# Performance work log

Measured on AMD Instinct MI355X. Metric: run time of the kernel, lower is better.

## Reference

```python
import jax, jax.numpy as jnp
import numpy as np

DIM = 512
NUM_HEADS = 8
HEAD_DIM = DIM // NUM_HEADS        # 64
L_HEADS = 4                        # int(8 * 0.5)
H_HEADS = NUM_HEADS - L_HEADS      # 4
L_DIM = L_HEADS * HEAD_DIM         # 256
H_DIM = H_HEADS * HEAD_DIM         # 256
WS = 2                             # window_size
SCALE = HEAD_DIM ** -0.5
SEQ_LEN = 1024


def setup_inputs() -> dict:
    key = jax.random.key(0)
    ks = jax.random.split(key, 13)
    B, N, C = 16, 1024, DIM
    def w(k, shape, fan_in):
        return (jax.random.normal(k, shape, jnp.float32) / np.sqrt(fan_in)).astype(jnp.float32)
    return {
        "x": jax.random.normal(ks[0], (B, N, C), jnp.float32),
        "pos_emb": jax.random.normal(ks[1], (1, SEQ_LEN, C), jnp.float32) * 0.02,
        "l_q_w": w(ks[2], (C, L_DIM), C),
        "l_kv_w": w(ks[3], (C, 2 * L_DIM), C),
        "l_proj_w": w(ks[4], (L_DIM, L_DIM), L_DIM),
        "l_proj_b": jax.random.normal(ks[5], (L_DIM,), jnp.float32) * 0.01,
        "h_qkv_w": w(ks[6], (C, 3 * H_DIM), C),
        "h_proj_w": w(ks[7], (H_DIM, H_DIM), H_DIM),
        "h_proj_b": jax.random.normal(ks[8], (H_DIM,), jnp.float32) * 0.01,
        "in_proj_w": w(ks[9], (C, 3 * C), C),
        "in_proj_b": jax.random.normal(ks[10], (3 * C,), jnp.float32) * 0.01,
        "out_proj_w": w(ks[11], (C, C), C),
        "out_proj_b": jax.random.normal(ks[12], (C,), jnp.float32) * 0.01,
        "H": 32,
        "W": 32,
    }


def _hifi(xg, h_qkv_w, h_proj_w, h_proj_b, H, W):
    B, _, _, C = xg.shape
    hg, wg = H // WS, W // WS
    G, T = hg * wg, WS * WS
    # [B, hg, WS, wg, WS, C] -> [B, G, T, C] (window partition)
    xw = xg.reshape(B, hg, WS, wg, WS, C).transpose(0, 1, 3, 2, 4, 5).reshape(B, G, T, C)
    qkv = (xw @ h_qkv_w).reshape(B, G, T, 3, H_HEADS, HEAD_DIM)
    q = qkv[:, :, :, 0].transpose(0, 1, 3, 2, 4)  # [B,G,h,T,d]
    k = qkv[:, :, :, 1].transpose(0, 1, 3, 2, 4)
    v = qkv[:, :, :, 2].transpose(0, 1, 3, 2, 4)
    attn = jax.nn.softmax(jnp.einsum("bghtd,bghsd->bghts", q, k) * SCALE, axis=-1)
    o = jnp.einsum("bghts,bghsd->bghtd", attn, v)
    # window un-partition: [B,G,h,T,d] -> [B,H,W,h_dim]
    o = o.transpose(0, 1, 3, 2, 4).reshape(B, hg, wg, WS, WS, H_DIM)
    o = o.transpose(0, 1, 3, 2, 4, 5).reshape(B, H, W, H_DIM)
    return o @ h_proj_w + h_proj_b


def _lofi(xg, l_q_w, l_kv_w, l_proj_w, l_proj_b, H, W):
    B, _, _, C = xg.shape
    N = H * W
    q = (xg @ l_q_w).reshape(B, N, L_HEADS, HEAD_DIM)
    kv = (xg @ l_kv_w).reshape(B, N, 2, L_HEADS, HEAD_DIM)
    k, v = kv[:, :, 0], kv[:, :, 1]
    attn = jax.nn.softmax(jnp.einsum("bnhd,bmhd->bhnm", q, k) * SCALE, axis=-1)
    o = jnp.einsum("bhnm,bmhd->bnhd", attn, v).reshape(B, H, W, L_DIM)
    return o @ l_proj_w + l_proj_b


def _mha(y, in_proj_w, in_proj_b, out_proj_w, out_proj_b):
    B, N, C = y.shape
    qkv = y @ in_proj_w + in_proj_b
    q, k, v = jnp.split(qkv, 3, axis=-1)
    q = q.reshape(B, N, NUM_HEADS, HEAD_DIM)
    k = k.reshape(B, N, NUM_HEADS, HEAD_DIM)
    v = v.reshape(B, N, NUM_HEADS, HEAD_DIM)
    attn = jax.nn.softmax(jnp.einsum("bnhd,bmhd->bhnm", q, k) * SCALE, axis=-1)
    o = jnp.einsum("bhnm,bmhd->bnhd", attn, v).reshape(B, N, C)
    return o @ out_proj_w + out_proj_b


def reference(x, pos_emb, l_q_w, l_kv_w, l_proj_w, l_proj_b,
              h_qkv_w, h_proj_w, h_proj_b,
              in_proj_w, in_proj_b, out_proj_w, out_proj_b, H, W):
    B, N, C = x.shape
    x = x + pos_emb[:, :N, :]
    xg = x.reshape(B, H, W, C)
    hifi_out = _hifi(xg, h_qkv_w, h_proj_w, h_proj_b, H, W)
    lofi_out = _lofi(xg, l_q_w, l_kv_w, l_proj_w, l_proj_b, H, W)
    y = jnp.concatenate([hifi_out, lofi_out], axis=-1).reshape(B, N, C)
    return _mha(y, in_proj_w, in_proj_b, out_proj_w, out_proj_b)
```

## Files before the change

### kernel.cpp

```cpp
#include <hip/hip_runtime.h>

typedef unsigned short ushort_t;
typedef short bf16x8 __attribute__((ext_vector_type(8)));
typedef float f32x4 __attribute__((ext_vector_type(4)));
typedef float f32x16 __attribute__((ext_vector_type(16)));

#define DEV __device__ __forceinline__

DEV ushort_t f2bf(float f) {
  return (ushort_t)((__float_as_uint(f) + 0x8000u) >> 16);
}
DEV unsigned pk_bf16(float lo, float hi) {
  unsigned a = __float_as_uint(lo) + 0x8000u;
  unsigned b = __float_as_uint(hi) + 0x8000u;
  return __builtin_amdgcn_perm(b, a, 0x07060302);
}
DEV unsigned cvtpk_bf16(float lo, float hi) {
  unsigned r;
  asm("v_cvt_pk_bf16_f32 %0, %1, %2" : "=v"(r) : "v"(lo), "v"(hi));
  return r;
}
DEV float bf2f(ushort_t h) {
  union { unsigned int u; float f; } v; v.u = ((unsigned int)h) << 16;
  return v.f;
}
DEV f32x4 mfma16(bf16x8 a, bf16x8 b, f32x4 c) {
  return __builtin_amdgcn_mfma_f32_16x16x32_bf16(a, b, c, 0, 0, 0);
}
DEV f32x16 mfma32(bf16x8 a, bf16x8 b, f32x16 c) {
  return __builtin_amdgcn_mfma_f32_32x32x16_bf16(a, b, c, 0, 0, 0);
}
DEV void pl32swap(unsigned &a, unsigned &b) {
  asm("v_permlane32_swap_b32 %0, %1" : "+v"(a), "+v"(b));
}
typedef __attribute__((address_space(3))) void lds_void;
typedef const __attribute__((address_space(1))) void glb_void;
DEV void gl_lds16(const void* g, void* l) {
  __builtin_amdgcn_global_load_lds((glb_void*)g, (lds_void*)l, 16, 0, 0);
}

__global__ __launch_bounds__(256)
void gemm_bt(const ushort_t* __restrict__ A, int lda,
             const ushort_t* __restrict__ BT,
             const float* __restrict__ bias,
             ushort_t* __restrict__ Cb, float* __restrict__ Cf,
             int ldc, int coff, int K, float scv, int sc_lo, int sc_hi)
{
  __shared__ __align__(16) ushort_t As[128 * 32];
  __shared__ __align__(16) ushort_t Bs[128 * 32];
  const int tid  = threadIdx.x;
  const int wave = tid >> 6, lane = tid & 63;
  const int quad = lane >> 4, r16 = lane & 15;
  const int nwg = gridDim.x * gridDim.y;
  const int lin = blockIdx.x + gridDim.x * blockIdx.y;
  const int logical = (lin & 7) * (nwg >> 3) + (lin >> 3);
  const int nbn = gridDim.y;
  const int mb = logical / nbn, nb = logical - mb * nbn;
  const int m0 = mb * 128, n0 = nb * 128;
  const int wm = (wave >> 1) * 64, wn = (wave & 1) * 64;

  f32x4 acc[4][4];
#pragma unroll
  for (int i = 0; i < 4; ++i)
#pragma unroll
    for (int j = 0; j < 4; ++j) acc[i][j] = (f32x4){0.f, 0.f, 0.f, 0.f};

  for (int kc = 0; kc < K; kc += 32) {
#pragma unroll
    for (int p = 0; p < 4; ++p) {
      int wp = p * 4 + wave;
      int lc = ((wp & 7) << 6) + lane;
      int row = lc >> 2, e8 = (lc & 3) * 8;
      if (wp < 8) gl_lds16(&A[(size_t)(m0 + row) * lda + kc + e8], &As[lc * 8]);
      else        gl_lds16(&BT[(size_t)(n0 + row) * K  + kc + e8], &Bs[lc * 8]);
    }
    __syncthreads();
    bf16x8 af[4], bfr[4];
#pragma unroll
    for (int i = 0; i < 4; ++i) {
      af[i]  = *(const bf16x8*)&As[(wm + i * 16 + r16) * 32 + quad * 8];
      bfr[i] = *(const bf16x8*)&Bs[(wn + i * 16 + r16) * 32 + quad * 8];
    }
#pragma unroll
    for (int mi = 0; mi < 4; ++mi)
#pragma unroll
      for (int ni = 0; ni < 4; ++ni)
        acc[mi][ni] = mfma16(af[mi], bfr[ni], acc[mi][ni]);
    __syncthreads();
  }

#pragma unroll
  for (int mi = 0; mi < 4; ++mi) {
#pragma unroll
    for (int ni = 0; ni < 4; ++ni) {
      int col = n0 + wn + ni * 16 + r16;
      float bv = bias ? bias[col] : 0.f;
      float s = (col >= sc_lo && col < sc_hi) ? scv : 1.0f;
#pragma unroll
      for (int r = 0; r < 4; ++r) {
        int row = m0 + wm + mi * 16 + quad * 4 + r;
        float v = (acc[mi][ni][r] + bv) * s;
        if (Cf) Cf[(size_t)row * ldc + coff + col] = v;
        else    Cb[(size_t)row * ldc + coff + col] = f2bf(v);
      }
    }
  }
}

__global__ __launch_bounds__(256)
void gemm_proj(const ushort_t* __restrict__ rB,
               const ushort_t* __restrict__ hT, const ushort_t* __restrict__ lT,
               const float* __restrict__ hb, const float* __restrict__ lb,
               ushort_t* __restrict__ y)
{
  __shared__ __align__(16) ushort_t As[128 * 32];
  __shared__ __align__(16) ushort_t Bs[128 * 32];
  const int tid  = threadIdx.x;
  const int wave = tid >> 6, lane = tid & 63;
  const int quad = lane >> 4, r16 = lane & 15;
  const int lin = blockIdx.x + 128 * blockIdx.y;
  const int logical = (lin & 7) * 64 + (lin >> 3);
  const int nidx = logical & 3, m0 = (logical >> 2) * 128;
  const int sel = nidx >> 1, n0 = (nidx & 1) * 128;
  const ushort_t* A  = rB + sel * 256;
  const ushort_t* BT = sel ? lT : hT;
  const float* bias  = sel ? lb : hb;
  const int coff = sel * 256;
  const int wm = (wave >> 1) * 64, wn = (wave & 1) * 64;

  f32x4 acc[4][4];
#pragma unroll
  for (int i = 0; i < 4; ++i)
#pragma unroll
    for (int j = 0; j < 4; ++j) acc[i][j] = (f32x4){0.f, 0.f, 0.f, 0.f};

  for (int kc = 0; kc < 256; kc += 32) {
#pragma unroll
    for (int p = 0; p < 4; ++p) {
      int wp = p * 4 + wave;
      int lc = ((wp & 7) << 6) + lane;
      int row = lc >> 2, e8 = (lc & 3) * 8;
      if (wp < 8) gl_lds16(&A[(size_t)(m0 + row) * 512 + kc + e8], &As[lc * 8]);
      else        gl_lds16(&BT[(size_t)(n0 + row) * 256 + kc + e8], &Bs[lc * 8]);
    }
    __syncthreads();
    bf16x8 af[4], bfr[4];
#pragma unroll
    for (int i = 0; i < 4; ++i) {
      af[i]  = *(const bf16x8*)&As[(wm + i * 16 + r16) * 32 + quad * 8];
      bfr[i] = *(const bf16x8*)&Bs[(wn + i * 16 + r16) * 32 + quad * 8];
    }
#pragma unroll
    for (int mi = 0; mi < 4; ++mi)
#pragma unroll
      for (int ni = 0; ni < 4; ++ni)
        acc[mi][ni] = mfma16(af[mi], bfr[ni], acc[mi][ni]);
    __syncthreads();
  }

#pragma unroll
  for (int mi = 0; mi < 4; ++mi) {
#pragma unroll
    for (int ni = 0; ni < 4; ++ni) {
      int col = n0 + wn + ni * 16 + r16;
      float bv = bias[col];
#pragma unroll
      for (int r = 0; r < 4; ++r) {
        int row = m0 + wm + mi * 16 + quad * 4 + r;
        y[(size_t)row * 512 + coff + col] = f2bf(acc[mi][ni][r] + bv);
      }
    }
  }
}

template<int QG>
__global__ __launch_bounds__(256, 2)
void flash_attn9(const ushort_t* __restrict__ Q, int qs, int q_ch,
                 const ushort_t* __restrict__ Kg, int ks, int k_ch,
                 const ushort_t* __restrict__ vT,
                 ushort_t* __restrict__ O, int os, int o_ch,
                 int N)
{
  __shared__ __align__(16) ushort_t Ks[2][64 * 64];
  __shared__ __align__(16) ushort_t Vs[2][64 * 64];

  const int H = gridDim.y;
  const int tid = threadIdx.x, wave = tid >> 6, lane = tid & 63;
  const int c = lane & 31, hh = lane >> 5;

  const int nwg = gridDim.x * H * gridDim.z;
  const int lin = blockIdx.x + gridDim.x * (blockIdx.y + H * blockIdx.z);
  const int logical = (lin & 7) * (nwg >> 3) + (lin >> 3);
  const int QBS = 8 / QG;
  const int qb = logical & (QBS - 1);
  const int t8 = logical / QBS;
  const int b = (H == 8) ? (t8 >> 3) : (t8 >> 2);
  const int h = t8 - b * H;
  const int q0 = qb * (128 * QG) + wave * (32 * QG);

  bf16x8 qf[QG][4];
#pragma unroll
  for (int qg = 0; qg < QG; ++qg) {
    const ushort_t* qp =
        Q + ((size_t)b * N + q0 + qg * 32 + c) * qs + q_ch + h * 64 + hh * 8;
#pragma unroll
    for (int s = 0; s < 4; ++s) qf[qg][s] = *(const bf16x8*)&qp[s * 16];
  }
  const ushort_t* kbase = Kg + ((size_t)b * N) * ks + k_ch + h * 64;
  const ushort_t* vbase = vT + ((size_t)(b * H + h) * 64) * N;

  f32x16 oacc[QG][2];
#pragma unroll
  for (int qg = 0; qg < QG; ++qg)
#pragma unroll
    for (int i = 0; i < 16; ++i) { oacc[qg][0][i] = 0.f; oacc[qg][1][i] = 0.f; }
  float l_acc[QG];
#pragma unroll
  for (int qg = 0; qg < QG; ++qg) l_acc[qg] = 0.f;

  auto stage = [&](int s0, int buf) {
#pragma unroll
    for (int p = 0; p < 4; ++p) {
      int wp = p * 4 + wave;
      int lc = ((wp & 7) << 6) + lane;
      int row = lc >> 3, cc = lc & 7;
      int e8 = ((cc ^ (row & 7)) * 8);
      if (wp < 8) gl_lds16(kbase + (size_t)(s0 + row) * ks + e8, &Ks[buf][lc * 8]);
      else        gl_lds16(vbase + (size_t)row * N + s0 + e8,    &Vs[buf][lc * 8]);
    }
  };

  stage(0, 0);
  const int NT = N >> 6;
  for (int it = 0; it < NT; ++it) {
    const int cur = it & 1;
    __syncthreads();
    if (it + 1 < NT) stage((it + 1) << 6, cur ^ 1);

    bf16x8 Bf[QG][4];
#pragma unroll
    for (int kb = 0; kb < 2; ++kb) {
      const int krow = kb * 32 + c;
      const ushort_t* kr = &Ks[cur][krow * 64];
      bf16x8 kf[4];
#pragma unroll
      for (int s = 0; s < 4; ++s)
        kf[s] = *(const bf16x8*)&kr[(((s << 1) + hh) ^ (krow & 7)) * 8];

#pragma unroll
      for (int qg = 0; qg < QG; ++qg) {
        f32x16 z;
#pragma unroll
        for (int i = 0; i < 16; ++i) z[i] = 0.f;
#pragma unroll
        for (int s = 0; s < 4; ++s) z = mfma32(kf[s], qf[qg][s], z);
        float ts = 0.f;
        unsigned W[8];
#pragma unroll
        for (int t = 0; t < 8; ++t) {
          float p0 = __builtin_amdgcn_exp2f(z[2 * t]);
          float p1 = __builtin_amdgcn_exp2f(z[2 * t + 1]);
          ts += p0 + p1;
          W[t] = cvtpk_bf16(p0, p1);
        }
        l_acc[qg] += ts;
        union U8 { bf16x8 f; unsigned u[4]; } f0, f1;
        unsigned a0 = W[0], b0 = W[2]; pl32swap(a0, b0);
        unsigned a1 = W[1], b1 = W[3]; pl32swap(a1, b1);
        f0.u[0] = a0; f0.u[1] = a1; f0.u[2] = b0; f0.u[3] = b1;
        unsigned a2 = W[4], b2 = W[6]; pl32swap(a2, b2);
        unsigned a3 = W[5], b3 = W[7]; pl32swap(a3, b3);
        f1.u[0] = a2; f1.u[1] = a3; f1.u[2] = b2; f1.u[3] = b3;
        Bf[qg][kb * 2]     = f0.f;
        Bf[qg][kb * 2 + 1] = f1.f;
      }
    }

#pragma unroll
    for (int db = 0; db < 2; ++db) {
      const int vrow = db * 32 + c;
      const ushort_t* vr = &Vs[cur][vrow * 64];
      bf16x8 vf[4];
#pragma unroll
      for (int s = 0; s < 4; ++s)
        vf[s] = *(const bf16x8*)&vr[(((s << 1) + hh) ^ (vrow & 7)) * 8];
#pragma unroll
      for (int qg = 0; qg < QG; ++qg)
#pragma unroll
        for (int s = 0; s < 4; ++s)
          oacc[qg][db] = mfma32(vf[s], Bf[qg][s], oacc[qg][db]);
    }
  }

#pragma unroll
  for (int qg = 0; qg < QG; ++qg) {
    float l = l_acc[qg] + __shfl_xor(l_acc[qg], 32);
    float inv = 1.f / l;
    ushort_t* op = O + ((size_t)b * N + q0 + qg * 32 + c) * os + o_ch + h * 64;
#pragma unroll
    for (int db = 0; db < 2; ++db) {
#pragma unroll
      for (int g = 0; g < 4; ++g) {
        uint2 pkv;
        pkv.x = cvtpk_bf16(oacc[qg][db][4 * g + 0] * inv, oacc[qg][db][4 * g + 1] * inv);
        pkv.y = cvtpk_bf16(oacc[qg][db][4 * g + 2] * inv, oacc[qg][db][4 * g + 3] * inv);
        *(uint2*)&op[db * 32 + g * 8 + hh * 4] = pkv;
      }
    }
  }
}

__global__ __launch_bounds__(256)
void transpose_v(const ushort_t* __restrict__ in, int ld, int ch,
                 ushort_t* __restrict__ out, int N, int H)
{
  __shared__ __align__(16) ushort_t T[64][72];
  const int s0 = blockIdx.x * 64, h = blockIdx.y, b = blockIdx.z;
  const int tid = threadIdx.x;
#pragma unroll
  for (int p = 0; p < 2; ++p) {
    int c = p * 256 + tid;
    int sr = c >> 3, d0 = (c & 7) * 8;
    *(uint4*)&T[sr][d0] =
        *(const uint4*)&in[((size_t)b * N + s0 + sr) * ld + ch + h * 64 + d0];
  }
  __syncthreads();
  const int d = tid >> 2, sp = (tid & 3) * 16;
  union { uint4 v; ushort_t u[8]; } A, B;
#pragma unroll
  for (int j = 0; j < 8; ++j) { A.u[j] = T[sp + j][d]; B.u[j] = T[sp + 8 + j][d]; }
  ushort_t* op = out + ((size_t)(b * H + h) * 64 + d) * N + s0 + sp;
  *(uint4*)&op[0] = A.v;
  *(uint4*)&op[8] = B.v;
}

__global__ __launch_bounds__(256)
void hifi_win(const ushort_t* __restrict__ qkv, int ld, ushort_t* __restrict__ out)
{
  const int bg = blockIdx.x;
  const int b = bg >> 8, g = bg & 255;
  const int head = threadIdx.x >> 6, lane = threadIdx.x & 63;
  const int gh = g >> 4, gw = g & 15;

  int n[4];
  float q[4], k[4], v[4];
#pragma unroll
  for (int t = 0; t < 4; ++t) {
    n[t] = (gh * 2 + (t >> 1)) * 32 + gw * 2 + (t & 1);
    size_t base = ((size_t)b * 1024 + n[t]) * ld + head * 64 + lane;
    q[t] = bf2f(qkv[base]);
    k[t] = bf2f(qkv[base + 256]);
    v[t] = bf2f(qkv[base + 512]);
  }
  float sc[4][4];
#pragma unroll
  for (int t = 0; t < 4; ++t)
#pragma unroll
    for (int s = 0; s < 4; ++s) {
      float p = q[t] * k[s];
#pragma unroll
      for (int off = 32; off >= 1; off >>= 1) p += __shfl_xor(p, off);
      sc[t][s] = p * 0.125f;
    }
#pragma unroll
  for (int t = 0; t < 4; ++t) {
    float m = fmaxf(fmaxf(sc[t][0], sc[t][1]), fmaxf(sc[t][2], sc[t][3]));
    float p0 = __expf(sc[t][0] - m), p1 = __expf(sc[t][1] - m);
    float p2 = __expf(sc[t][2] - m), p3 = __expf(sc[t][3] - m);
    float sum = p0 + p1 + p2 + p3;
    float o = (p0 * v[0] + p1 * v[1] + p2 * v[2] + p3 * v[3]) / sum;
    out[((size_t)b * 1024 + n[t]) * 512 + head * 64 + lane] = f2bf(o);
  }
}

struct WEnt { const float* W; ushort_t* WT; int K; int N; };
struct WArgs { WEnt e[7]; };

__global__ __launch_bounds__(256)
void w_prep(WArgs a)
{
  WEnt w = a.e[blockIdx.z];
  if ((int)blockIdx.x >= (w.K >> 6) || (int)blockIdx.y >= (w.N >> 6)) return;
  __shared__ float T[64][65];
  const int k0 = blockIdx.x * 64, n0 = blockIdx.y * 64;
  const int tid = threadIdx.x;
#pragma unroll
  for (int p = 0; p < 4; ++p) {
    int c = p * 256 + tid;
    int kr = c >> 4, f4 = (c & 15) * 4;
    float4 v = *(const float4*)&w.W[(size_t)(k0 + kr) * w.N + n0 + f4];
    T[f4 + 0][kr] = v.x; T[f4 + 1][kr] = v.y;
    T[f4 + 2][kr] = v.z; T[f4 + 3][kr] = v.w;
  }
  __syncthreads();
  const int nl = tid >> 2, kp = (tid & 3) * 16;
  union { uint4 v; ushort_t u[8]; } A, B;
#pragma unroll
  for (int j = 0; j < 8; ++j) {
    A.u[j] = f2bf(T[nl][kp + j]);
    B.u[j] = f2bf(T[nl][kp + 8 + j]);
  }
  ushort_t* op = w.WT + (size_t)(n0 + nl) * w.K + k0 + kp;
  *(uint4*)&op[0] = A.v;
  *(uint4*)&op[8] = B.v;
}

__global__ void add_pos(const float* __restrict__ x, const float* __restrict__ pos,
                        ushort_t* __restrict__ xpe)
{
  int idx = blockIdx.x * 256 + threadIdx.x;
  int e = idx * 4;
  float4 xv = *(const float4*)&x[e];
  float4 pv = *(const float4*)&pos[e & (512 * 1024 - 1)];
  uint2 pk;
  pk.x = pk_bf16(xv.x + pv.x, xv.y + pv.y);
  pk.y = pk_bf16(xv.z + pv.z, xv.w + pv.w);
  *(uint2*)&xpe[e] = pk;
}

extern "C" void kernel_launch(void* const* d_in, const int* in_sizes, int n_in,
                              void* d_out, int out_size, void* d_ws, size_t ws_size,
                              hipStream_t stream)
{
  const float* x         = (const float*)d_in[0];
  const float* pos       = (const float*)d_in[1];
  const float* l_q_w     = (const float*)d_in[2];
  const float* l_kv_w    = (const float*)d_in[3];
  const float* l_proj_w  = (const float*)d_in[4];
  const float* l_proj_b  = (const float*)d_in[5];
  const float* h_qkv_w   = (const float*)d_in[6];
  const float* h_proj_w  = (const float*)d_in[7];
  const float* h_proj_b  = (const float*)d_in[8];
  const float* in_proj_w = (const float*)d_in[9];
  const float* in_proj_b = (const float*)d_in[10];
  const float* out_proj_w= (const float*)d_in[11];
  const float* out_proj_b= (const float*)d_in[12];
  float* out = (float*)d_out;

  const float QSCALE = 0.125f * 1.44269504f;

  char* ws = (char*)d_ws;
  ushort_t* xpe = (ushort_t*)(ws);
  ushort_t* y   = (ushort_t*)(ws + (size_t)16777216);
  ushort_t* F   = (ushort_t*)(ws + (size_t)33554432);
  ushort_t* rB  = (ushort_t*)(ws + (size_t)83886080);
  ushort_t* wb  = (ushort_t*)(ws + (size_t)100663296);

  ushort_t* F_T      = wb;
  ushort_t* h_projT  = wb + 786432;
  ushort_t* l_projT  = wb + 851968;
  ushort_t* in_projT = wb + 917504;
  ushort_t* out_projT= wb + 1703936;

  const int M = 16384;
  ushort_t* vT_lo = xpe;
  ushort_t* vT_m  = rB;

  WArgs wa;
  wa.e[0] = {h_qkv_w,   F_T,                 512, 768};
  wa.e[1] = {l_q_w,     F_T + 768 * 512,     512, 256};
  wa.e[2] = {l_kv_w,    F_T + 1024 * 512,    512, 512};
  wa.e[3] = {h_proj_w,  h_projT,             256, 256};
  wa.e[4] = {l_proj_w,  l_projT,             256, 256};
  wa.e[5] = {in_proj_w, in_projT,            512, 1536};
  wa.e[6] = {out_proj_w,out_projT,           512, 512};
  w_prep<<<dim3(8, 24, 7), dim3(256), 0, stream>>>(wa);

  add_pos<<<dim3(8192), dim3(256), 0, stream>>>(x, pos, xpe);

  gemm_bt<<<dim3(M / 128, 12), dim3(256), 0, stream>>>(
      xpe, 512, F_T, nullptr, F, nullptr, 1536, 0, 512, QSCALE, 768, 1024);
  hifi_win<<<dim3(4096), dim3(256), 0, stream>>>(F, 1536, rB);
  transpose_v<<<dim3(16, 4, 16), dim3(256), 0, stream>>>(
      F, 1536, 1280, vT_lo, 1024, 4);
  flash_attn9<1><<<dim3(8, 4, 16), dim3(256), 0, stream>>>(
      F, 1536, 768, F, 1536, 1024, vT_lo, rB, 512, 256, 1024);
  gemm_proj<<<dim3(128, 4), dim3(256), 0, stream>>>(
      rB, h_projT, l_projT, h_proj_b, l_proj_b, y);
  gemm_bt<<<dim3(M / 128, 12), dim3(256), 0, stream>>>(
      y, 512, in_projT, in_proj_b, F, nullptr, 1536, 0, 512, QSCALE, 0, 512);
  transpose_v<<<dim3(16, 8, 16), dim3(256), 0, stream>>>(
      F, 1536, 1024, vT_m, 1024, 8);
  flash_attn9<2><<<dim3(4, 8, 16), dim3(256), 0, stream>>>(
      F, 1536, 0, F, 1536, 512, vT_m, xpe, 512, 0, 1024);
  gemm_bt<<<dim3(M / 128, 4), dim3(256), 0, stream>>>(
      xpe, 512, out_projT, out_proj_b, nullptr, out, 512, 0, 512, 1.0f, 0, 0);
}
```

Before: 313.7 us.

## Double-buffer GEMM LDS tiles and vectorize epilogue stores via swapped MFMA operands

Both GEMM kernels now use two LDS buffers, issuing the global-to-LDS load for the next K chunk before computing on the current one, which removes one barrier per iteration and overlaps load latency with MFMA work. The MFMA operands are swapped so each lane holds four consecutive columns of one row. The epilogue can then load the bias as a float4 and write packed bf16 or float4 stores instead of scattered scalar stores. This doubles LDS use per block, which may lower occupancy, and rounding switches to the hardware v_cvt_pk_bf16 instruction.

```diff
diff --git a/kernel.cpp b/kernel.cpp
--- a/kernel.cpp
+++ b/kernel.cpp
@@ -46,8 +46,8 @@
              ushort_t* __restrict__ Cb, float* __restrict__ Cf,
              int ldc, int coff, int K, float scv, int sc_lo, int sc_hi)
 {
-  __shared__ __align__(16) ushort_t As[128 * 32];
-  __shared__ __align__(16) ushort_t Bs[128 * 32];
+  __shared__ __align__(16) ushort_t As[2][128 * 32];
+  __shared__ __align__(16) ushort_t Bs[2][128 * 32];
   const int tid  = threadIdx.x;
   const int wave = tid >> 6, lane = tid & 63;
   const int quad = lane >> 4, r16 = lane & 15;
@@ -65,43 +65,58 @@
 #pragma unroll
     for (int j = 0; j < 4; ++j) acc[i][j] = (f32x4){0.f, 0.f, 0.f, 0.f};
 
-  for (int kc = 0; kc < K; kc += 32) {
+  auto stage = [&](int kc, int buf) {
 #pragma unroll
     for (int p = 0; p < 4; ++p) {
       int wp = p * 4 + wave;
       int lc = ((wp & 7) << 6) + lane;
       int row = lc >> 2, e8 = (lc & 3) * 8;
-      if (wp < 8) gl_lds16(&A[(size_t)(m0 + row) * lda + kc + e8], &As[lc * 8]);
-      else        gl_lds16(&BT[(size_t)(n0 + row) * K  + kc + e8], &Bs[lc * 8]);
-    }
+      if (wp < 8) gl_lds16(&A[(size_t)(m0 + row) * lda + kc + e8], &As[buf][lc * 8]);
+      else        gl_lds16(&BT[(size_t)(n0 + row) * K  + kc + e8], &Bs[buf][lc * 8]);
+    }
+  };
+
+  stage(0, 0);
+  const int NI = K >> 5;
+  for (int ki = 0; ki < NI; ++ki) {
+    const int cur = ki & 1;
     __syncthreads();
+    if (ki + 1 < NI) stage((ki + 1) << 5, cur ^ 1);
     bf16x8 af[4], bfr[4];
 #pragma unroll
     for (int i = 0; i < 4; ++i) {
-      af[i]  = *(const bf16x8*)&As[(wm + i * 16 + r16) * 32 + quad * 8];
-      bfr[i] = *(const bf16x8*)&Bs[(wn + i * 16 + r16) * 32 + quad * 8];
+      af[i]  = *(const bf16x8*)&As[cur][(wm + i * 16 + r16) * 32 + quad * 8];
+      bfr[i] = *(const bf16x8*)&Bs[cur][(wn + i * 16 + r16) * 32 + quad * 8];
     }
 #pragma unroll
     for (int mi = 0; mi < 4; ++mi)
 #pragma unroll
       for (int ni = 0; ni < 4; ++ni)
-        acc[mi][ni] = mfma16(af[mi], bfr[ni], acc[mi][ni]);
-    __syncthreads();
+        acc[mi][ni] = mfma16(bfr[ni], af[mi], acc[mi][ni]);
   }
 
 #pragma unroll
   for (int mi = 0; mi < 4; ++mi) {
+    const int row = m0 + wm + mi * 16 + r16;
 #pragma unroll
     for (int ni = 0; ni < 4; ++ni) {
-      int col = n0 + wn + ni * 16 + r16;
-      float bv = bias ? bias[col] : 0.f;
-      float s = (col >= sc_lo && col < sc_hi) ? scv : 1.0f;
+      const int col = n0 + wn + ni * 16 + quad * 4;
+      float4 bv = bias ? *(const float4*)&bias[col]
+                       : make_float4(0.f, 0.f, 0.f, 0.f);
+      float v[4];
 #pragma unroll
       for (int r = 0; r < 4; ++r) {
-        int row = m0 + wm + mi * 16 + quad * 4 + r;
-        float v = (acc[mi][ni][r] + bv) * s;
-        if (Cf) Cf[(size_t)row * ldc + coff + col] = v;
-        else    Cb[(size_t)row * ldc + coff + col] = f2bf(v);
+        float s = (col + r >= sc_lo && col + r < sc_hi) ? scv : 1.0f;
+        v[r] = (acc[mi][ni][r] + (&bv.x)[r]) * s;
+      }
+      if (Cf) {
+        *(float4*)&Cf[(size_t)row * ldc + coff + col] =
+            make_float4(v[0], v[1], v[2], v[3]);
+      } else {
+        uint2 pk;
+        pk.x = cvtpk_bf16(v[0], v[1]);
+        pk.y = cvtpk_bf16(v[2], v[3]);
+        *(uint2*)&Cb[(size_t)row * ldc + coff + col] = pk;
       }
     }
   }
@@ -113,8 +128,8 @@
                const float* __restrict__ hb, const float* __restrict__ lb,
                ushort_t* __restrict__ y)
 {
-  __shared__ __align__(16) ushort_t As[128 * 32];
-  __shared__ __align__(16) ushort_t Bs[128 * 32];
+  __shared__ __align__(16) ushort_t As[2][128 * 32];
+  __shared__ __align__(16) ushort_t Bs[2][128 * 32];
   const int tid  = threadIdx.x;
   const int wave = tid >> 6, lane = tid & 63;
   const int quad = lane >> 4, r16 = lane & 15;
@@ -134,41 +149,46 @@
 #pragma unroll
     for (int j = 0; j < 4; ++j) acc[i][j] = (f32x4){0.f, 0.f, 0.f, 0.f};
 
-  for (int kc = 0; kc < 256; kc += 32) {
+  auto stage = [&](int kc, int buf) {
 #pragma unroll
     for (int p = 0; p < 4; ++p) {
       int wp = p * 4 + wave;
       int lc = ((wp & 7) << 6) + lane;
       int row = lc >> 2, e8 = (lc & 3) * 8;
-      if (wp < 8) gl_lds16(&A[(size_t)(m0 + row) * 512 + kc + e8], &As[lc * 8]);
-      else        gl_lds16(&BT[(size_t)(n0 + row) * 256 + kc + e8], &Bs[lc * 8]);
-    }
+      if (wp < 8) gl_lds16(&A[(size_t)(m0 + row) * 512 + kc + e8], &As[buf][lc * 8]);
+      else        gl_lds16(&BT[(size_t)(n0 + row) * 256 + kc + e8], &Bs[buf][lc * 8]);
+    }
+  };
+
+  stage(0, 0);
+  for (int ki = 0; ki < 8; ++ki) {
+    const int cur = ki & 1;
     __syncthreads();
+    if (ki + 1 < 8) stage((ki + 1) << 5, cur ^ 1);
     bf16x8 af[4], bfr[4];
 #pragma unroll
     for (int i = 0; i < 4; ++i) {
-      af[i]  = *(const bf16x8*)&As[(wm + i * 16 + r16) * 32 + quad * 8];
-      bfr[i] = *(const bf16x8*)&Bs[(wn + i * 16 + r16) * 32 + quad * 8];
+      af[i]  = *(const bf16x8*)&As[cur][(wm + i * 16 + r16) * 32 + quad * 8];
+      bfr[i] = *(const bf16x8*)&Bs[cur][(wn + i * 16 + r16) * 32 + quad * 8];
     }
 #pragma unroll
     for (int mi = 0; mi < 4; ++mi)
 #pragma unroll
       for (int ni = 0; ni < 4; ++ni)
-        acc[mi][ni] = mfma16(af[mi], bfr[ni], acc[mi][ni]);
-    __syncthreads();
+        acc[mi][ni] = mfma16(bfr[ni], af[mi], acc[mi][ni]);
   }
 
 #pragma unroll
   for (int mi = 0; mi < 4; ++mi) {
+    const int row = m0 + wm + mi * 16 + r16;
 #pragma unroll
     for (int ni = 0; ni < 4; ++ni) {
-      int col = n0 + wn + ni * 16 + r16;
-      float bv = bias[col];
-#pragma unroll
-      for (int r = 0; r < 4; ++r) {
-        int row = m0 + wm + mi * 16 + quad * 4 + r;
-        y[(size_t)row * 512 + coff + col] = f2bf(acc[mi][ni][r] + bv);
-      }
+      const int col = n0 + wn + ni * 16 + quad * 4;
+      float4 bv = *(const float4*)&bias[col];
+      uint2 pk;
+      pk.x = cvtpk_bf16(acc[mi][ni][0] + bv.x, acc[mi][ni][1] + bv.y);
+      pk.y = cvtpk_bf16(acc[mi][ni][2] + bv.z, acc[mi][ni][3] + bv.w);
+      *(uint2*)&y[(size_t)row * 512 + coff + col] = pk;
     }
   }
 }
```

New measurement: 332.7 us. 6.0% more time.
